# Optimization experiments

Hardware: AMD Instinct MI355X
Metric: run time of the kernel (lower is better)

Reference implementation:

```python
import jax, jax.numpy as jnp
from jax import lax
import numpy as np

B, S, E, HID = 16, 7, 64, 64
RES = (64, 64); D = RES[0] * RES[1]
XLOW, XHIGH = -0.5, 0.5
RLOW, RHIGH = float(np.sqrt(0.01)), float(np.sqrt(0.05))
PIXEL_MULT = 1.0; N_ITER = 3; TSOFT = 1.0 / float(np.sqrt(E))

def _build_grid():
    ranges = [np.linspace(XLOW, XHIGH, r) for r in RES]
    g = np.stack(np.meshgrid(*ranges, indexing='xy'), axis=-1)
    g = g.reshape(RES[0], RES[1], -1).reshape(1, -1, 2)
    return jnp.asarray(g, dtype=jnp.float32)

ABS_GRID = _build_grid()  # [1, D, 2]

def _ln(x, g, b):
    m = jnp.mean(x, -1, keepdims=True)
    v = jnp.mean(jnp.square(x - m), -1, keepdims=True)
    return (x - m) * lax.rsqrt(v + 1e-5) * g + b

def _forward(data, slot_noise, pos_rand, conv0_w, conv0_b, conv1_w, conv1_b, conv2_w, conv2_b,
             dataN_g, dataN_b, queryN_g, queryN_b, toK_w, toK_b, toV_w, toV_b, dense_w, dense_b,
             mlp1_w, mlp1_b, mlp2_w, mlp2_b, gru_wih, gru_whh, gru_bih, gru_bhh,
             alpha1_w, alpha1_b, alpha2_w, alpha2_b, final1_w, final1_b, final2_w, final2_b,
             slots_mu, slots_logsigma):
    dn = ('NCHW', 'OIHW', 'NCHW')
    def conv(x, w, b):
        return lax.conv_general_dilated(x, w, (1, 1), 'SAME', dimension_numbers=dn) + b[None, :, None, None]
    # CNN encoder: Conv-ReLU x3, 'same' padding, k=5
    x = jax.nn.relu(conv(data, conv0_w, conv0_b))
    x = jax.nn.relu(conv(x, conv1_w, conv1_b))
    x = jax.nn.relu(conv(x, conv2_w, conv2_b))
    enc = x.transpose(0, 2, 3, 1).reshape(B, D, HID)
    enc = _ln(enc, dataN_g, dataN_b)

    queries = slots_mu + jnp.exp(slots_logsigma) * slot_noise  # [B,S,E]
    # init_slots: faithful replication (source indexes the SLOT dim, and swaps rlow/rhigh)
    pos_scale = pos_rand.at[:, :2, :].add(-0.5)
    pos_scale = pos_scale.at[:, -1, :].set((RLOW - RHIGH) * pos_rand[:, -1, :] + RHIGH)

    encK = enc @ toK_w + toK_b  # [B,D,E]
    encV = enc @ toV_w + toV_b

    def init_mlp(y):
        y = _ln(y, queryN_g, queryN_b)
        return jax.nn.relu(y @ mlp1_w + mlp1_b) @ mlp2_w + mlp2_b

    def get_kv(ps):
        # per-slot relative grid: [B,S,D,2]
        rel = (ABS_GRID[:, None] - ps[:, :, None, :2]) / ps[:, :, -1][:, :, None, None]
        eg = PIXEL_MULT * (rel @ dense_w + dense_b)  # [B,S,D,E]
        return init_mlp(encK[:, None] + eg), init_mlp(encV[:, None] + eg)

    def att_wts(q, k):
        logits = jnp.einsum('bse,bsde->bsd', q, k) * TSOFT
        att = jax.nn.softmax(logits, axis=1)  # softmax over slots
        wts = att / jnp.sum(att, -1, keepdims=True) + 1e-8
        return att, wts

    def update_frames(wts):
        new_pos = jnp.einsum('bsd,de->bse', wts, ABS_GRID[0])  # [B,S,2]
        d2 = jnp.sum(jnp.square(ABS_GRID[:, None] - new_pos[:, :, None]), -1)  # [B,S,D]
        new_scale = jnp.sqrt(jnp.einsum('bsd,bsd->bs', wts, d2))
        return jnp.concatenate([new_pos, new_scale[..., None]], -1)

    def gru(xg, h):
        gi = xg @ gru_wih.T + gru_bih
        gh = h @ gru_whh.T + gru_bhh
        ir, iz, inn = jnp.split(gi, 3, -1)
        hr, hz, hn = jnp.split(gh, 3, -1)
        r = jax.nn.sigmoid(ir + hr)
        z = jax.nn.sigmoid(iz + hz)
        n = jnp.tanh(inn + r * hn)
        return (1.0 - z) * n + z * h

    for _ in range(N_ITER):
        keys, vals = get_kv(pos_scale)
        att, wts = att_wts(_ln(queries, queryN_g, queryN_b), keys)
        pos_scale = update_frames(wts)
        upd = jnp.einsum('bsd,bsde->bse', wts, vals)
        queries = gru(upd.reshape(-1, E), queries.reshape(-1, E)).reshape(B, S, E)

    keys, _ = get_kv(pos_scale)
    att, wts = att_wts(_ln(queries, queryN_g, queryN_b), keys)
    nps = update_frames(wts)
    alpha = jax.nn.sigmoid(jax.nn.relu(queries @ alpha1_w + alpha1_b) @ alpha2_w + alpha2_b)
    slot_feat = jax.nn.relu(queries @ final1_w + final1_b) @ final2_w + final2_b + nps
    return queries, att, slot_feat, alpha

def setup_inputs() -> dict:
    ks = jax.random.split(jax.random.key(0), 20)
    f32 = jnp.float32
    def rn(i, shape, s):
        return jax.random.normal(ks[i], shape, f32) * s
    inp = dict(
        data=jax.random.normal(ks[0], (B, 1, RES[0], RES[1]), f32),
        slot_noise=jax.random.normal(ks[1], (B, S, E), f32),
        pos_rand=jax.random.uniform(ks[2], (B, S, 3), dtype=f32),
        conv0_w=rn(3, (HID, 1, 5, 5), 0.2), conv0_b=jnp.zeros(HID, f32),
        conv1_w=rn(4, (HID, HID, 5, 5), 0.025), conv1_b=jnp.zeros(HID, f32),
        conv2_w=rn(5, (HID, HID, 5, 5), 0.025), conv2_b=jnp.zeros(HID, f32),
        dataN_g=jnp.ones(HID, f32), dataN_b=jnp.zeros(HID, f32),
        queryN_g=jnp.ones(E, f32), queryN_b=jnp.zeros(E, f32),
        toK_w=rn(6, (HID, E), 0.125), toK_b=jnp.zeros(E, f32),
        toV_w=rn(7, (HID, E), 0.125), toV_b=jnp.zeros(E, f32),
        dense_w=rn(8, (2, E), 0.7), dense_b=jnp.zeros(E, f32),
        mlp1_w=rn(9, (E, E), 0.125), mlp1_b=jnp.zeros(E, f32),
        mlp2_w=rn(10, (E, E), 0.125), mlp2_b=jnp.zeros(E, f32),
        gru_wih=rn(11, (3 * E, E), 0.125), gru_whh=rn(12, (3 * E, E), 0.125),
        gru_bih=jnp.zeros(3 * E, f32), gru_bhh=jnp.zeros(3 * E, f32),
        alpha1_w=rn(13, (E, 32), 0.125), alpha1_b=jnp.zeros(32, f32),
        alpha2_w=rn(14, (32, 1), 0.18), alpha2_b=jnp.zeros(1, f32),
        final1_w=rn(15, (E, HID), 0.125), final1_b=jnp.zeros(HID, f32),
        final2_w=rn(16, (HID, 3), 0.125), final2_b=jnp.zeros(3, f32),
        slots_mu=rn(17, (1, 1, E), 1.0),
        slots_logsigma=rn(18, (1, 1, E), 0.01),
    )
    return inp

def reference(data, slot_noise, pos_rand, conv0_w, conv0_b, conv1_w, conv1_b, conv2_w, conv2_b,
              dataN_g, dataN_b, queryN_g, queryN_b, toK_w, toK_b, toV_w, toV_b, dense_w, dense_b,
              mlp1_w, mlp1_b, mlp2_w, mlp2_b, gru_wih, gru_whh, gru_bih, gru_bhh,
              alpha1_w, alpha1_b, alpha2_w, alpha2_b, final1_w, final1_b, final2_w, final2_b,
              slots_mu, slots_logsigma):
    return _forward(data, slot_noise, pos_rand, conv0_w, conv0_b, conv1_w, conv1_b, conv2_w, conv2_b,
                    dataN_g, dataN_b, queryN_g, queryN_b, toK_w, toK_b, toV_w, toV_b, dense_w, dense_b,
                    mlp1_w, mlp1_b, mlp2_w, mlp2_b, gru_wih, gru_whh, gru_bih, gru_bhh,
                    alpha1_w, alpha1_b, alpha2_w, alpha2_b, final1_w, final1_b, final2_w, final2_b,
                    slots_mu, slots_logsigma)
```

## Files before the change

### kernel.cpp

```cpp
#include <hip/hip_runtime.h>
#include <cmath>


#define RLOW_F 0.1f
#define RHIGH_F 0.22360679774997896f

typedef __attribute__((ext_vector_type(8))) __bf16 bf16x8;
typedef __attribute__((ext_vector_type(4))) float f32x4;

__device__ __forceinline__ float wsum64(float v){
  #pragma unroll
  for (int off = 32; off > 0; off >>= 1) v += __shfl_xor(v, off, 64);
  return v;
}
__device__ __forceinline__ float rdlane(float v, int l){
  return __int_as_float(__builtin_amdgcn_readlane(__float_as_int(v), l));
}
__device__ __forceinline__ unsigned short bf16bits(float v){
  __bf16 h = (__bf16)v;
  return *reinterpret_cast<unsigned short*>(&h);
}

__device__ __forceinline__ void pp_core(int row, int e, float qv,
    float px, float py, float sc,
    const float* __restrict__ qg_, const float* __restrict__ qb_,
    const float* __restrict__ dw, const float* __restrict__ db,
    const float* __restrict__ mlp2w, const float* __restrict__ mlp2b,
    float* __restrict__ absc, float* __restrict__ w2qc,
    float* __restrict__ sum_att){
  float m = wsum64(qv) * (1.f/64.f);
  float d = qv - m;
  float var = wsum64(d*d) * (1.f/64.f);
  float qlnv = d * (1.0f/sqrtf(var + 1e-5f)) * qg_[e] + qb_[e];
  float A  = dw[e]      / sc;
  float Bv = dw[64 + e] / sc;
  absc[row*192 + e]       = A;
  absc[row*192 + 64 + e]  = Bv;
  absc[row*192 + 128 + e] = db[e] - px*A - py*Bv;
  float acc = 0.f;
  const float* wrow = mlp2w + e*64;
  for (int j = 0; j < 64; j++) acc = fmaf(wrow[j], rdlane(qlnv, j), acc);
  w2qc[row*68 + e] = acc;
  float c2 = wsum64(mlp2b[e] * qlnv);
  if (e == 0){ w2qc[row*68 + 64] = c2; sum_att[row] = 0.f; }
}

__global__ void k_prep(const float* __restrict__ noise, const float* __restrict__ prand,
                       const float* __restrict__ mu, const float* __restrict__ logsig,
                       const float* __restrict__ qg_, const float* __restrict__ qb_,
                       const float* __restrict__ dw, const float* __restrict__ db,
                       const float* __restrict__ mlp2w, const float* __restrict__ mlp2b,
                       float* __restrict__ queries, float* __restrict__ ps,
                       float* __restrict__ absc, float* __restrict__ w2qc,
                       float* __restrict__ sum_att, float* __restrict__ upd){
  int row = blockIdx.x;
  int e = threadIdx.x;
  int s = row % 7;
  float qv = mu[e] + expf(logsig[e]) * noise[row*64 + e];
  queries[row*64 + e] = qv;
  upd[row*64 + e] = 0.f;
  float pv = 0.f;
  if (e < 3){
    float pr = prand[row*3 + e];
    if (s < 2)       pv = pr - 0.5f;
    else if (s == 6) pv = (RLOW_F - RHIGH_F)*pr + RHIGH_F;
    else             pv = pr;
    ps[row*3 + e] = pv;
  }
  float px = rdlane(pv, 0), py = rdlane(pv, 1), sc = rdlane(pv, 2);
  pp_core(row, e, qv, px, py, sc, qg_, qb_, dw, db, mlp2w, mlp2b,
          absc, w2qc, sum_att);
}

__global__ __launch_bounds__(256) void k_conv0(const float* __restrict__ in,
                        const float* __restrict__ w, const float* __restrict__ bias,
                        unsigned short* __restrict__ out){
  int bi = blockIdx.x; int b = bi >> 6; int y = bi & 63;
  int t = threadIdx.x; int lane = t & 63; int xg = t >> 6;
  __shared__ float s_in[5*68];
  __shared__ float s_w[64*25];
  __shared__ float s_out[64*65];
  for (int i = t; i < 1600; i += 256) s_w[i] = w[i];
  for (int i = t; i < 340; i += 256){
    int r = i / 68, cx = i % 68;
    int yy = y + r - 2, gx = cx - 2;
    float v = 0.f;
    if (yy >= 0 && yy < 64 && gx >= 0 && gx < 64) v = in[(b*64 + yy)*64 + gx];
    s_in[r*68 + cx] = v;
  }
  __syncthreads();
  int o = lane;
  float bv = bias[o];
  float acc[16];
  #pragma unroll
  for (int k = 0; k < 16; k++) acc[k] = bv;
  #pragma unroll
  for (int ky = 0; ky < 5; ky++){
    float rv[20];
    const float4* p = reinterpret_cast<const float4*>(&s_in[ky*68 + xg*16]);
    #pragma unroll
    for (int q = 0; q < 5; q++){ float4 f = p[q]; rv[q*4]=f.x; rv[q*4+1]=f.y; rv[q*4+2]=f.z; rv[q*4+3]=f.w; }
    #pragma unroll
    for (int kx = 0; kx < 5; kx++){
      float wv = s_w[o*25 + ky*5 + kx];
      #pragma unroll
      for (int k = 0; k < 16; k++) acc[k] = fmaf(rv[k+kx], wv, acc[k]);
    }
  }
  #pragma unroll
  for (int k = 0; k < 16; k++) s_out[o*65 + xg*16 + k] = fmaxf(acc[k], 0.f);
  __syncthreads();
  for (int i = t; i < 4096; i += 256){
    int px = i >> 6, ch = i & 63;
    out[((size_t)(b*64 + y)*64 + px)*64 + ch] = bf16bits(s_out[ch*65 + px]);
  }
}

__global__ void k_packconv(const float* __restrict__ w, unsigned short* __restrict__ out){
  int idx = blockIdx.x*256 + threadIdx.x;
  if (idx >= 102400) return;
  int j = idx & 7;
  int l = (idx >> 3) & 63;
  int frag = idx >> 9;
  int nt = frag & 3;
  int ks = (frag >> 2) % 10;
  int dy = frag / 40;
  int q = l >> 4, cr = l & 15;
  int k = ks*32 + q*8 + j;
  int kx = k >> 6, ch = k & 63;
  int n = nt*16 + cr;
  out[idx] = bf16bits(w[((n*64 + ch)*5 + dy)*5 + kx]);
}

__global__ __launch_bounds__(256) void k_convm(const unsigned short* __restrict__ in_bf,
                        const unsigned short* __restrict__ wpack,
                        const float* __restrict__ bias,
                        const float* __restrict__ lng, const float* __restrict__ lnb,
                        unsigned short* __restrict__ out_bf, float* __restrict__ out_f,
                        int mode){
  int bi = blockIdx.x;
  int b = bi >> 4; int yg = bi & 15;
  int t = threadIdx.x; int wv = t >> 6; int l = t & 63;
  int q = l >> 4, cr = l & 15;
  int p0 = wv*16;

  __shared__ char lds[8*68*144];

  for (int ri = 0; ri < 8; ri++){
    int yy = yg*4 + ri - 2;
    bool rok = (yy >= 0 && yy < 64);
    const uint4* src = reinterpret_cast<const uint4*>(in_bf + (size_t)(b*64 + yy)*64*64);
    for (int i = t; i < 544; i += 256){
      int px = i >> 3, c8 = i & 7;
      uint4 v = {0u,0u,0u,0u};
      int gx = px - 2;
      if (rok && gx >= 0 && gx < 64) v = src[gx*8 + c8];
      *reinterpret_cast<uint4*>(&lds[ri*9792 + px*144 + c8*16]) = v;
    }
  }
  __syncthreads();

  f32x4 acc[4][4];
  #pragma unroll
  for (int r = 0; r < 4; r++)
    #pragma unroll
    for (int nt = 0; nt < 4; nt++) acc[r][nt] = (f32x4){0.f,0.f,0.f,0.f};

  const bf16x8* wp = reinterpret_cast<const bf16x8*>(wpack);
  for (int dy = 0; dy < 5; dy++){
    for (int ks = 0; ks < 10; ks++){
      bf16x8 Bf[4];
      int fbase = (dy*10 + ks)*4;
      #pragma unroll
      for (int nt = 0; nt < 4; nt++) Bf[nt] = wp[(fbase + nt)*64 + l];
      int aoff = (p0 + cr + (ks >> 1))*144 + (ks & 1)*64 + q*16;
      #pragma unroll
      for (int r = 0; r < 4; r++){
        bf16x8 a = *reinterpret_cast<const bf16x8*>(&lds[(r + dy)*9792 + aoff]);
        #pragma unroll
        for (int nt = 0; nt < 4; nt++)
          acc[r][nt] = __builtin_amdgcn_mfma_f32_16x16x32_bf16(a, Bf[nt], acc[r][nt], 0, 0, 0);
      }
    }
  }

  float bv[4];
  #pragma unroll
  for (int nt = 0; nt < 4; nt++) bv[nt] = bias[nt*16 + cr];

  if (mode == 0){
    #pragma unroll
    for (int r = 0; r < 4; r++){
      int y = yg*4 + r;
      #pragma unroll
      for (int reg = 0; reg < 4; reg++){
        int p = p0 + q*4 + reg;
        size_t base = ((size_t)(b*64 + y)*64 + p)*64;
        #pragma unroll
        for (int nt = 0; nt < 4; nt++)
          out_bf[base + nt*16 + cr] = bf16bits(fmaxf(acc[r][nt][reg] + bv[nt], 0.f));
      }
    }
  } else {
    float gv[4], bb[4];
    #pragma unroll
    for (int nt = 0; nt < 4; nt++){ gv[nt] = lng[nt*16 + cr]; bb[nt] = lnb[nt*16 + cr]; }
    #pragma unroll
    for (int r = 0; r < 4; r++){
      int y = yg*4 + r;
      #pragma unroll
      for (int reg = 0; reg < 4; reg++){
        int p = p0 + q*4 + reg;
        float v[4]; float s1 = 0.f, s2 = 0.f;
        #pragma unroll
        for (int nt = 0; nt < 4; nt++){
          v[nt] = fmaxf(acc[r][nt][reg] + bv[nt], 0.f);
          s1 += v[nt]; s2 += v[nt]*v[nt];
        }
        #pragma unroll
        for (int m = 1; m < 16; m <<= 1){ s1 += __shfl_xor(s1, m, 64); s2 += __shfl_xor(s2, m, 64); }
        float mean = s1 * (1.f/64.f);
        float var  = s2 * (1.f/64.f) - mean*mean;
        float rstd = 1.0f/sqrtf(var + 1e-5f);
        size_t base = ((size_t)b*4096 + y*64 + p)*64;
        #pragma unroll
        for (int nt = 0; nt < 4; nt++)
          out_f[base + nt*16 + cr] = (v[nt] - mean)*rstd*gv[nt] + bb[nt];
      }
    }
  }
}

__global__ void k_packw1(const float* __restrict__ w1, unsigned short* __restrict__ out){
  int idx = blockIdx.x*256 + threadIdx.x;
  int jj = idx & 7;
  int lane = (idx >> 3) & 63;
  int frag = idx >> 9;
  int ks = frag >> 2, nt = frag & 3;
  int q = lane >> 4, cr = lane & 15;
  int k = ks*32 + q*8 + jj;
  int n = nt*16 + cr;
  out[idx] = bf16bits(w1[k*64 + n]);
}

__global__ __launch_bounds__(256) void k_projm(const float* __restrict__ enc,
                       const unsigned short* __restrict__ kpack, const float* __restrict__ bk,
                       const unsigned short* __restrict__ vpack, const float* __restrict__ bvp,
                       float* __restrict__ K, float* __restrict__ V){
  int bi = blockIdx.x; int b = bi >> 6; int tile = bi & 63;
  int t = threadIdx.x; int wv = t >> 6; int l = t & 63;
  int q = l >> 4, cr = l & 15;
  int d0 = tile*64 + wv*16;

  const bf16x8* kp = reinterpret_cast<const bf16x8*>(kpack);
  const bf16x8* vp = reinterpret_cast<const bf16x8*>(vpack);
  bf16x8 KB[8], VB[8];
  #pragma unroll
  for (int f = 0; f < 8; f++){ KB[f] = kp[f*64 + l]; VB[f] = vp[f*64 + l]; }

  const float* er = enc + (size_t)(b*4096 + d0 + cr)*64;
  bf16x8 a0, a1;
  #pragma unroll
  for (int h = 0; h < 2; h++){
    const float4* e4 = reinterpret_cast<const float4*>(er + (h ? (32 + q*8) : (q*8)));
    #pragma unroll
    for (int p = 0; p < 2; p++){
      float4 e = e4[p];
      if (h == 0){ a0[p*4+0]=(__bf16)e.x; a0[p*4+1]=(__bf16)e.y; a0[p*4+2]=(__bf16)e.z; a0[p*4+3]=(__bf16)e.w; }
      else       { a1[p*4+0]=(__bf16)e.x; a1[p*4+1]=(__bf16)e.y; a1[p*4+2]=(__bf16)e.z; a1[p*4+3]=(__bf16)e.w; }
    }
  }

  f32x4 zero = {0.f,0.f,0.f,0.f};
  f32x4 aK[4], aV[4];
  #pragma unroll
  for (int nt = 0; nt < 4; nt++){
    aK[nt] = __builtin_amdgcn_mfma_f32_16x16x32_bf16(a0, KB[nt],     zero,   0, 0, 0);
    aK[nt] = __builtin_amdgcn_mfma_f32_16x16x32_bf16(a1, KB[4 + nt], aK[nt], 0, 0, 0);
    aV[nt] = __builtin_amdgcn_mfma_f32_16x16x32_bf16(a0, VB[nt],     zero,   0, 0, 0);
    aV[nt] = __builtin_amdgcn_mfma_f32_16x16x32_bf16(a1, VB[4 + nt], aV[nt], 0, 0, 0);
  }
  #pragma unroll
  for (int nt = 0; nt < 4; nt++){
    float bkv = bk[nt*16 + cr], bvv = bvp[nt*16 + cr];
    #pragma unroll
    for (int reg = 0; reg < 4; reg++){
      size_t base = ((size_t)b*4096 + d0 + q*4 + reg)*64 + nt*16 + cr;
      K[base] = aK[nt][reg] + bkv;
      V[base] = aV[nt][reg] + bvv;
    }
  }
}

__global__ __launch_bounds__(256) void k_attnK(const float* __restrict__ encX,
     const unsigned short* __restrict__ w1pack, const float* __restrict__ mlp1b,
     const float* __restrict__ absc, const float* __restrict__ qg_,
     const float* __restrict__ qb_, const float* __restrict__ w2qc,
     float* __restrict__ att, float* __restrict__ sum_att){
  int bi = blockIdx.x;
  int b = bi >> 6, tile = bi & 63;
  int t = threadIdx.x; int wv = t >> 6; int l = t & 63;
  int q = l >> 4, cr = l & 15;
  int m0 = tile*64 + wv*16;
  int drow = m0 + cr;

  __shared__ float s_log[7*64];
  __shared__ float s_absc[7*192];
  __shared__ float s_wq[7*68];
  for (int i = t; i < 1344; i += 256) s_absc[i] = absc[b*7*192 + i];
  for (int i = t; i < 476;  i += 256) s_wq[i]   = w2qc[b*7*68 + i];

  const bf16x8* wp = reinterpret_cast<const bf16x8*>(w1pack);
  bf16x8 Bf[8];
  #pragma unroll
  for (int f = 0; f < 8; f++) Bf[f] = wp[f*64 + l];

  const float* er = encX + (size_t)(b*4096 + drow)*64;
  float gx = -0.5f + (float)(drow & 63) * (1.f/63.f);
  float gy = -0.5f + (float)((drow >> 6) & 63) * (1.f/63.f);
  float xb[16], gq[16], bq[16];
  #pragma unroll
  for (int h = 0; h < 2; h++){
    int fb = h ? (32 + q*8) : (q*8);
    const float4* e4 = reinterpret_cast<const float4*>(er + fb);
    const float4* g4 = reinterpret_cast<const float4*>(qg_ + fb);
    const float4* b4 = reinterpret_cast<const float4*>(qb_ + fb);
    #pragma unroll
    for (int p = 0; p < 2; p++){
      float4 e = e4[p], gg = g4[p], bb = b4[p];
      int o = h*8 + p*4;
      xb[o+0]=e.x; xb[o+1]=e.y; xb[o+2]=e.z; xb[o+3]=e.w;
      gq[o+0]=gg.x; gq[o+1]=gg.y; gq[o+2]=gg.z; gq[o+3]=gg.w;
      bq[o+0]=bb.x; bq[o+1]=bb.y; bq[o+2]=bb.z; bq[o+3]=bb.w;
    }
  }
  float b1v[4];
  #pragma unroll
  for (int nt = 0; nt < 4; nt++) b1v[nt] = mlp1b[nt*16 + cr];
  __syncthreads();

  for (int s = 0; s < 7; s++){
    const float* Ac = s_absc + s*192;
    float x[16];
    #pragma unroll
    for (int h = 0; h < 2; h++){
      int fb = h ? (32 + q*8) : (q*8);
      const float4* A4 = reinterpret_cast<const float4*>(Ac + fb);
      const float4* B4 = reinterpret_cast<const float4*>(Ac + 64 + fb);
      const float4* C4 = reinterpret_cast<const float4*>(Ac + 128 + fb);
      #pragma unroll
      for (int p = 0; p < 2; p++){
        float4 Av = A4[p], Bv = B4[p], Cv = C4[p];
        int o = h*8 + p*4;
        x[o+0] = xb[o+0] + gx*Av.x + gy*Bv.x + Cv.x;
        x[o+1] = xb[o+1] + gx*Av.y + gy*Bv.y + Cv.y;
        x[o+2] = xb[o+2] + gx*Av.z + gy*Bv.z + Cv.z;
        x[o+3] = xb[o+3] + gx*Av.w + gy*Bv.w + Cv.w;
      }
    }
    float sum = 0.f;
    #pragma unroll
    for (int k = 0; k < 16; k++) sum += x[k];
    sum += __shfl_xor(sum, 16, 64); sum += __shfl_xor(sum, 32, 64);
    float m = sum * (1.f/64.f);
    float v = 0.f;
    #pragma unroll
    for (int k = 0; k < 16; k++){ float dd = x[k] - m; v += dd*dd; }
    v += __shfl_xor(v, 16, 64); v += __shfl_xor(v, 32, 64);
    float rstd = 1.0f/sqrtf(v * (1.f/64.f) + 1e-5f);

    bf16x8 a0, a1;
    #pragma unroll
    for (int k = 0; k < 8; k++)  a0[k] = (__bf16)((x[k]   - m)*rstd*gq[k]   + bq[k]);
    #pragma unroll
    for (int k = 0; k < 8; k++)  a1[k] = (__bf16)((x[8+k] - m)*rstd*gq[8+k] + bq[8+k]);

    f32x4 zero = {0.f, 0.f, 0.f, 0.f};
    f32x4 acc[4];
    #pragma unroll
    for (int nt = 0; nt < 4; nt++){
      acc[nt] = __builtin_amdgcn_mfma_f32_16x16x32_bf16(a0, Bf[nt],     zero,    0, 0, 0);
      acc[nt] = __builtin_amdgcn_mfma_f32_16x16x32_bf16(a1, Bf[4 + nt], acc[nt], 0, 0, 0);
    }

    float c2 = s_wq[s*68 + 64];
    float p[4] = {0.f, 0.f, 0.f, 0.f};
    #pragma unroll
    for (int nt = 0; nt < 4; nt++){
      float wqv = s_wq[s*68 + nt*16 + cr];
      #pragma unroll
      for (int reg = 0; reg < 4; reg++){
        float y = fmaxf(acc[nt][reg] + b1v[nt], 0.f);
        p[reg] = fmaf(y, wqv, p[reg]);
      }
    }
    #pragma unroll
    for (int reg = 0; reg < 4; reg++){
      #pragma unroll
      for (int off = 1; off < 16; off <<= 1) p[reg] += __shfl_xor(p[reg], off, 64);
    }
    if (cr == 0){
      #pragma unroll
      for (int reg = 0; reg < 4; reg++)
        s_log[s*64 + wv*16 + q*4 + reg] = (p[reg] + c2) * 0.125f;
    }
  }
  __syncthreads();

  if (t < 64){
    float lv[7];
    #pragma unroll
    for (int s = 0; s < 7; s++) lv[s] = s_log[s*64 + t];
    float mx = lv[0];
    #pragma unroll
    for (int s = 1; s < 7; s++) mx = fmaxf(mx, lv[s]);
    float sm = 0.f;
    #pragma unroll
    for (int s = 0; s < 7; s++){ lv[s] = expf(lv[s] - mx); sm += lv[s]; }
    float inv = 1.0f / sm;
    for (int s = 0; s < 7; s++){
      float a = lv[s] * inv;
      att[(size_t)(b*7+s)*4096 + tile*64 + t] = a;
      float ws = wsum64(a);
      if (t == 0) atomicAdd(&sum_att[b*7+s], ws);
    }
  }
}

__global__ __launch_bounds__(256) void k_attnV(const float* __restrict__ encX,
     const unsigned short* __restrict__ w1pack, const float* __restrict__ mlp1b,
     const float* __restrict__ absc, const float* __restrict__ qg_,
     const float* __restrict__ qb_, const float* __restrict__ att,
     const float* __restrict__ sum_att, float* __restrict__ upd){
  int bi = blockIdx.x;
  int b = bi >> 6, tile = bi & 63;
  int t = threadIdx.x; int wv = t >> 6; int l = t & 63;
  int q = l >> 4, cr = l & 15;
  int m0 = tile*64 + wv*16;
  int drow = m0 + cr;

  __shared__ float s_absc[7*192];
  __shared__ float s_att[7*64];
  __shared__ float s_upd[7*64];
  __shared__ float s_inv[7];
  for (int i = t; i < 1344; i += 256) s_absc[i] = absc[b*7*192 + i];
  for (int i = t; i < 448;  i += 256){
    s_att[i] = att[(size_t)(b*7 + (i >> 6))*4096 + tile*64 + (i & 63)];
    s_upd[i] = 0.f;
  }
  if (t < 7) s_inv[t] = 1.0f / sum_att[b*7 + t];

  const bf16x8* wp = reinterpret_cast<const bf16x8*>(w1pack);
  bf16x8 Bf[8];
  #pragma unroll
  for (int f = 0; f < 8; f++) Bf[f] = wp[f*64 + l];

  const float* er = encX + (size_t)(b*4096 + drow)*64;
  float gx = -0.5f + (float)(drow & 63) * (1.f/63.f);
  float gy = -0.5f + (float)((drow >> 6) & 63) * (1.f/63.f);
  float xb[16], gq[16], bq[16];
  #pragma unroll
  for (int h = 0; h < 2; h++){
    int fb = h ? (32 + q*8) : (q*8);
    const float4* e4 = reinterpret_cast<const float4*>(er + fb);
    const float4* g4 = reinterpret_cast<const float4*>(qg_ + fb);
    const float4* b4 = reinterpret_cast<const float4*>(qb_ + fb);
    #pragma unroll
    for (int p = 0; p < 2; p++){
      float4 e = e4[p], gg = g4[p], bb = b4[p];
      int o = h*8 + p*4;
      xb[o+0]=e.x; xb[o+1]=e.y; xb[o+2]=e.z; xb[o+3]=e.w;
      gq[o+0]=gg.x; gq[o+1]=gg.y; gq[o+2]=gg.z; gq[o+3]=gg.w;
      bq[o+0]=bb.x; bq[o+1]=bb.y; bq[o+2]=bb.z; bq[o+3]=bb.w;
    }
  }
  float b1v[4];
  #pragma unroll
  for (int nt = 0; nt < 4; nt++) b1v[nt] = mlp1b[nt*16 + cr];
  __syncthreads();

  for (int s = 0; s < 7; s++){
    const float* Ac = s_absc + s*192;
    float x[16];
    #pragma unroll
    for (int h = 0; h < 2; h++){
      int fb = h ? (32 + q*8) : (q*8);
      const float4* A4 = reinterpret_cast<const float4*>(Ac + fb);
      const float4* B4 = reinterpret_cast<const float4*>(Ac + 64 + fb);
      const float4* C4 = reinterpret_cast<const float4*>(Ac + 128 + fb);
      #pragma unroll
      for (int p = 0; p < 2; p++){
        float4 Av = A4[p], Bv = B4[p], Cv = C4[p];
        int o = h*8 + p*4;
        x[o+0] = xb[o+0] + gx*Av.x + gy*Bv.x + Cv.x;
        x[o+1] = xb[o+1] + gx*Av.y + gy*Bv.y + Cv.y;
        x[o+2] = xb[o+2] + gx*Av.z + gy*Bv.z + Cv.z;
        x[o+3] = xb[o+3] + gx*Av.w + gy*Bv.w + Cv.w;
      }
    }
    float sum = 0.f;
    #pragma unroll
    for (int k = 0; k < 16; k++) sum += x[k];
    sum += __shfl_xor(sum, 16, 64); sum += __shfl_xor(sum, 32, 64);
    float m = sum * (1.f/64.f);
    float v = 0.f;
    #pragma unroll
    for (int k = 0; k < 16; k++){ float dd = x[k] - m; v += dd*dd; }
    v += __shfl_xor(v, 16, 64); v += __shfl_xor(v, 32, 64);
    float rstd = 1.0f/sqrtf(v * (1.f/64.f) + 1e-5f);

    bf16x8 a0, a1;
    #pragma unroll
    for (int k = 0; k < 8; k++)  a0[k] = (__bf16)((x[k]   - m)*rstd*gq[k]   + bq[k]);
    #pragma unroll
    for (int k = 0; k < 8; k++)  a1[k] = (__bf16)((x[8+k] - m)*rstd*gq[8+k] + bq[8+k]);

    f32x4 zero = {0.f, 0.f, 0.f, 0.f};
    f32x4 acc[4];
    #pragma unroll
    for (int nt = 0; nt < 4; nt++){
      acc[nt] = __builtin_amdgcn_mfma_f32_16x16x32_bf16(a0, Bf[nt],     zero,    0, 0, 0);
      acc[nt] = __builtin_amdgcn_mfma_f32_16x16x32_bf16(a1, Bf[4 + nt], acc[nt], 0, 0, 0);
    }

    float rsa = s_inv[s];
    float wr[4];
    #pragma unroll
    for (int reg = 0; reg < 4; reg++)
      wr[reg] = fmaf(s_att[s*64 + wv*16 + q*4 + reg], rsa, 1e-8f);
    float pc[4];
    #pragma unroll
    for (int nt = 0; nt < 4; nt++){
      pc[nt] = 0.f;
      #pragma unroll
      for (int reg = 0; reg < 4; reg++)
        pc[nt] = fmaf(wr[reg], fmaxf(acc[nt][reg] + b1v[nt], 0.f), pc[nt]);
    }
    #pragma unroll
    for (int nt = 0; nt < 4; nt++){
      pc[nt] += __shfl_xor(pc[nt], 16, 64);
      pc[nt] += __shfl_xor(pc[nt], 32, 64);
    }
    if (q == 0){
      #pragma unroll
      for (int nt = 0; nt < 4; nt++)
        atomicAdd(&s_upd[s*64 + nt*16 + cr], pc[nt]);
    }
  }
  __syncthreads();
  for (int i = t; i < 448; i += 256)
    atomicAdd(&upd[b*448 + i], s_upd[i]);
}

__global__ void k_frames(const float* __restrict__ att, const float* __restrict__ sum_att,
                         float* __restrict__ psout, float* __restrict__ sumw){
  int bs = blockIdx.x; int t = threadIdx.x;
  float sa = sum_att[bs];
  float a0 = 0.f, ax = 0.f, ay = 0.f, a2 = 0.f;
  for (int d = t; d < 4096; d += 256){
    float wv = att[bs*4096 + d] / sa + 1e-8f;
    float gx = -0.5f + (float)(d & 63) * (1.f/63.f);
    float gy = -0.5f + (float)(d >> 6) * (1.f/63.f);
    a0 += wv; ax += wv*gx; ay += wv*gy; a2 += wv*(gx*gx + gy*gy);
  }
  __shared__ float red[4][4];
  int lane = t & 63, w = t >> 6;
  a0 = wsum64(a0); ax = wsum64(ax); ay = wsum64(ay); a2 = wsum64(a2);
  if (lane == 0){ red[w][0]=a0; red[w][1]=ax; red[w][2]=ay; red[w][3]=a2; }
  __syncthreads();
  if (t == 0){
    float W0=0,Wx=0,Wy=0,Wg=0;
    for (int k = 0; k < 4; k++){ W0+=red[k][0]; Wx+=red[k][1]; Wy+=red[k][2]; Wg+=red[k][3]; }
    float s2 = Wg - (Wx*Wx + Wy*Wy)*(2.f - W0);
    psout[bs*3+0] = Wx; psout[bs*3+1] = Wy; psout[bs*3+2] = sqrtf(fmaxf(s2, 0.f));
    sumw[bs] = W0;
  }
}

__global__ void k_gru(float* __restrict__ upd, float* __restrict__ queries,
                      const float* __restrict__ wih, const float* __restrict__ whh,
                      const float* __restrict__ bih, const float* __restrict__ bhh,
                      const float* __restrict__ mlp2w, const float* __restrict__ mlp2b,
                      const float* __restrict__ sumw, const float* __restrict__ ps,
                      const float* __restrict__ qg_, const float* __restrict__ qb_,
                      const float* __restrict__ dw, const float* __restrict__ db,
                      float* __restrict__ absc, float* __restrict__ w2qc,
                      float* __restrict__ sum_att){
  int row = blockIdx.x; int t = threadIdx.x;
  __shared__ float us[64], hs[64], xs[64], gis[192], ghs[192];
  if (t < 64){ us[t] = upd[row*64 + t]; hs[t] = queries[row*64 + t]; }
  __syncthreads();
  if (t < 64){
    float a = sumw[row] * mlp2b[t];
    for (int i = 0; i < 64; i++) a = fmaf(us[i], mlp2w[i*64 + t], a);
    xs[t] = a;
  }
  __syncthreads();
  float gi = bih[t], gh = bhh[t];
  for (int e = 0; e < 64; e++){
    gi = fmaf(wih[t*64 + e], xs[e], gi);
    gh = fmaf(whh[t*64 + e], hs[e], gh);
  }
  gis[t] = gi; ghs[t] = gh;
  __syncthreads();
  if (t < 64){
    float r = 1.0f/(1.0f + expf(-(gis[t]      + ghs[t])));
    float z = 1.0f/(1.0f + expf(-(gis[64+t]   + ghs[64+t])));
    float n = tanhf(gis[128+t] + r*ghs[128+t]);
    float newq = (1.0f - z)*n + z*hs[t];
    queries[row*64 + t] = newq;
    upd[row*64 + t] = 0.f;
    float px = ps[row*3], py = ps[row*3+1], sc = ps[row*3+2];
    pp_core(row, t, newq, px, py, sc, qg_, qb_, dw, db, mlp2w, mlp2b,
            absc, w2qc, sum_att);
  }
}

__global__ void k_final(const float* __restrict__ queries, const float* __restrict__ nps,
                        const float* __restrict__ a1w, const float* __restrict__ a1b,
                        const float* __restrict__ a2w, const float* __restrict__ a2b,
                        const float* __restrict__ f1w, const float* __restrict__ f1b,
                        const float* __restrict__ f2w, const float* __restrict__ f2b,
                        float* __restrict__ out){
  int bs = blockIdx.x; int e = threadIdx.x;
  __shared__ float qs[64], hf[64], ha[32];
  float q = queries[bs*64 + e];
  qs[e] = q;
  out[bs*64 + e] = q;
  __syncthreads();
  float accf = f1b[e];
  for (int i = 0; i < 64; i++) accf = fmaf(qs[i], f1w[i*64 + e], accf);
  hf[e] = fmaxf(accf, 0.f);
  if (e < 32){
    float acca = a1b[e];
    for (int i = 0; i < 64; i++) acca = fmaf(qs[i], a1w[i*32 + e], acca);
    ha[e] = fmaxf(acca, 0.f);
  }
  __syncthreads();
  if (e < 3){
    float sf = f2b[e];
    for (int o = 0; o < 64; o++) sf = fmaf(hf[o], f2w[o*3 + e], sf);
    out[465920 + bs*3 + e] = sf + nps[bs*3 + e];
  }
  if (e == 32){
    float al = a2b[0];
    for (int o = 0; o < 32; o++) al = fmaf(ha[o], a2w[o], al);
    out[466256 + bs] = 1.0f/(1.0f + expf(-al));
  }
}

extern "C" void kernel_launch(void* const* d_in, const int* in_sizes, int n_in,
                              void* d_out, int out_size, void* d_ws, size_t ws_size,
                              hipStream_t stream){
  const float* data        = (const float*)d_in[0];
  const float* slot_noise  = (const float*)d_in[1];
  const float* pos_rand    = (const float*)d_in[2];
  const float* conv0_w     = (const float*)d_in[3];
  const float* conv0_b     = (const float*)d_in[4];
  const float* conv1_w     = (const float*)d_in[5];
  const float* conv1_b     = (const float*)d_in[6];
  const float* conv2_w     = (const float*)d_in[7];
  const float* conv2_b     = (const float*)d_in[8];
  const float* dataN_g     = (const float*)d_in[9];
  const float* dataN_b     = (const float*)d_in[10];
  const float* queryN_g    = (const float*)d_in[11];
  const float* queryN_b    = (const float*)d_in[12];
  const float* toK_w       = (const float*)d_in[13];
  const float* toK_b       = (const float*)d_in[14];
  const float* toV_w       = (const float*)d_in[15];
  const float* toV_b       = (const float*)d_in[16];
  const float* dense_w     = (const float*)d_in[17];
  const float* dense_b     = (const float*)d_in[18];
  const float* mlp1_w      = (const float*)d_in[19];
  const float* mlp1_b      = (const float*)d_in[20];
  const float* mlp2_w      = (const float*)d_in[21];
  const float* mlp2_b      = (const float*)d_in[22];
  const float* gru_wih     = (const float*)d_in[23];
  const float* gru_whh     = (const float*)d_in[24];
  const float* gru_bih     = (const float*)d_in[25];
  const float* gru_bhh     = (const float*)d_in[26];
  const float* alpha1_w    = (const float*)d_in[27];
  const float* alpha1_b    = (const float*)d_in[28];
  const float* alpha2_w    = (const float*)d_in[29];
  const float* alpha2_b    = (const float*)d_in[30];
  const float* final1_w    = (const float*)d_in[31];
  const float* final1_b    = (const float*)d_in[32];
  const float* final2_w    = (const float*)d_in[33];
  const float* final2_b    = (const float*)d_in[34];
  const float* slots_mu    = (const float*)d_in[35];
  const float* slots_lsig  = (const float*)d_in[36];

  float* ws   = (float*)d_ws;
  float* bufA = ws;
  float* bufB = bufA + 4194304;
  float* bufC = bufB + 4194304;
  float* attw = bufC + 4194304;
  float* queries = attw + 458752;
  float* ps   = queries + 7168;
  float* absc = ps + 512;
  float* sum_att = absc + 21504;
  float* upd  = sum_att + 128;
  float* nps  = upd + 7168;
  float* w2qc = nps + 512;
  float* sumw = w2qc + 7616;
  unsigned short* w1pack = (unsigned short*)(sumw + 128);
  unsigned short* kpack  = w1pack + 4096;
  unsigned short* vpack  = kpack + 4096;
  unsigned short* wp1    = vpack + 4096;
  unsigned short* wp2    = wp1 + 102400;

  unsigned short* c0_bf = (unsigned short*)bufA;
  unsigned short* c1_bf = (unsigned short*)bufC;
  float* enc  = bufB;
  float* encK = bufA;
  float* encV = bufC;

  float* outq   = (float*)d_out;
  float* outatt = outq + 7168;

  k_prep<<<112, 64, 0, stream>>>(slot_noise, pos_rand, slots_mu, slots_lsig,
                                 queryN_g, queryN_b, dense_w, dense_b, mlp2_w, mlp2_b,
                                 queries, ps, absc, w2qc, sum_att, upd);
  k_packw1<<<16, 256, 0, stream>>>(mlp1_w, w1pack);
  k_packw1<<<16, 256, 0, stream>>>(toK_w, kpack);
  k_packw1<<<16, 256, 0, stream>>>(toV_w, vpack);
  k_packconv<<<400, 256, 0, stream>>>(conv1_w, wp1);
  k_packconv<<<400, 256, 0, stream>>>(conv2_w, wp2);
  k_conv0<<<1024, 256, 0, stream>>>(data, conv0_w, conv0_b, c0_bf);
  k_convm<<<256, 256, 0, stream>>>(c0_bf, wp1, conv1_b, nullptr, nullptr, c1_bf, nullptr, 0);
  k_convm<<<256, 256, 0, stream>>>(c1_bf, wp2, conv2_b, dataN_g, dataN_b, nullptr, enc, 1);
  k_projm<<<1024, 256, 0, stream>>>(enc, kpack, toK_b, vpack, toV_b, encK, encV);

  for (int p = 0; p < 4; p++){
    float* attp = (p == 3) ? outatt : attw;
    k_attnK<<<1024, 256, 0, stream>>>(encK, w1pack, mlp1_b, absc, queryN_g, queryN_b,
                                      w2qc, attp, sum_att);
    k_frames<<<112, 256, 0, stream>>>(attp, sum_att, (p == 3) ? nps : ps, sumw);
    if (p < 3){
      k_attnV<<<1024, 256, 0, stream>>>(encV, w1pack, mlp1_b, absc, queryN_g, queryN_b,
                                        attp, sum_att, upd);
      k_gru<<<112, 192, 0, stream>>>(upd, queries, gru_wih, gru_whh, gru_bih, gru_bhh,
                                     mlp2_w, mlp2_b, sumw, ps, queryN_g, queryN_b,
                                     dense_w, dense_b, absc, w2qc, sum_att);
    }
  }
  k_final<<<112, 64, 0, stream>>>(queries, nps, alpha1_w, alpha1_b, alpha2_w, alpha2_b,
                                  final1_w, final1_b, final2_w, final2_b, outq);
}
```

Before: 565.7 us.

## Fuse frame-moment reduction into attention kernel and store K/V in bf16

Removes the separate k_frames kernel. k_attnK now reduces the per-slot weighted moments (sum, x, y, r^2) within each block and accumulates them with atomics. The new slot position and scale are computed analytically in k_gru and k_final, and W0 and the 1e-8 term become closed-form constants. Encoded K and V are also stored as bf16, which halves the bytes the attention kernels read on every iteration. The cost is bf16 rounding of K/V, a reformulated reduction with a different summation order, and hardcoded constants that depend on the grid resolution.

```diff
diff --git a/kernel.cpp b/kernel.cpp
--- a/kernel.cpp
+++ b/kernel.cpp
@@ -4,6 +4,8 @@
 
 #define RLOW_F 0.1f
 #define RHIGH_F 0.22360679774997896f
+#define W0CONST 1.00004096f
+#define SR2 704.3386243f
 
 typedef __attribute__((ext_vector_type(8))) __bf16 bf16x8;
 typedef __attribute__((ext_vector_type(4))) float f32x4;
@@ -26,8 +28,7 @@
     const float* __restrict__ qg_, const float* __restrict__ qb_,
     const float* __restrict__ dw, const float* __restrict__ db,
     const float* __restrict__ mlp2w, const float* __restrict__ mlp2b,
-    float* __restrict__ absc, float* __restrict__ w2qc,
-    float* __restrict__ sum_att){
+    float* __restrict__ absc, float* __restrict__ w2qc){
   float m = wsum64(qv) * (1.f/64.f);
   float d = qv - m;
   float var = wsum64(d*d) * (1.f/64.f);
@@ -42,7 +43,7 @@
   for (int j = 0; j < 64; j++) acc = fmaf(wrow[j], rdlane(qlnv, j), acc);
   w2qc[row*68 + e] = acc;
   float c2 = wsum64(mlp2b[e] * qlnv);
-  if (e == 0){ w2qc[row*68 + 64] = c2; sum_att[row] = 0.f; }
+  if (e == 0) w2qc[row*68 + 64] = c2;
 }
 
 __global__ void k_prep(const float* __restrict__ noise, const float* __restrict__ prand,
@@ -52,13 +53,14 @@
                        const float* __restrict__ mlp2w, const float* __restrict__ mlp2b,
                        float* __restrict__ queries, float* __restrict__ ps,
                        float* __restrict__ absc, float* __restrict__ w2qc,
-                       float* __restrict__ sum_att, float* __restrict__ upd){
+                       float* __restrict__ accF, float* __restrict__ upd){
   int row = blockIdx.x;
   int e = threadIdx.x;
   int s = row % 7;
   float qv = mu[e] + expf(logsig[e]) * noise[row*64 + e];
   queries[row*64 + e] = qv;
   upd[row*64 + e] = 0.f;
+  if (e < 4) accF[row*4 + e] = 0.f;
   float pv = 0.f;
   if (e < 3){
     float pr = prand[row*3 + e];
@@ -68,8 +70,7 @@
     ps[row*3 + e] = pv;
   }
   float px = rdlane(pv, 0), py = rdlane(pv, 1), sc = rdlane(pv, 2);
-  pp_core(row, e, qv, px, py, sc, qg_, qb_, dw, db, mlp2w, mlp2b,
-          absc, w2qc, sum_att);
+  pp_core(row, e, qv, px, py, sc, qg_, qb_, dw, db, mlp2w, mlp2b, absc, w2qc);
 }
 
 __global__ __launch_bounds__(256) void k_conv0(const float* __restrict__ in,
@@ -90,10 +91,10 @@
   }
   __syncthreads();
   int o = lane;
-  float bv = bias[o];
+  float bvv = bias[o];
   float acc[16];
   #pragma unroll
-  for (int k = 0; k < 16; k++) acc[k] = bv;
+  for (int k = 0; k < 16; k++) acc[k] = bvv;
   #pragma unroll
   for (int ky = 0; ky < 5; ky++){
     float rv[20];
@@ -184,9 +185,9 @@
     }
   }
 
-  float bv[4];
-  #pragma unroll
-  for (int nt = 0; nt < 4; nt++) bv[nt] = bias[nt*16 + cr];
+  float bvv[4];
+  #pragma unroll
+  for (int nt = 0; nt < 4; nt++) bvv[nt] = bias[nt*16 + cr];
 
   if (mode == 0){
     #pragma unroll
@@ -198,7 +199,7 @@
         size_t base = ((size_t)(b*64 + y)*64 + p)*64;
         #pragma unroll
         for (int nt = 0; nt < 4; nt++)
-          out_bf[base + nt*16 + cr] = bf16bits(fmaxf(acc[r][nt][reg] + bv[nt], 0.f));
+          out_bf[base + nt*16 + cr] = bf16bits(fmaxf(acc[r][nt][reg] + bvv[nt], 0.f));
       }
     }
   } else {
@@ -214,7 +215,7 @@
         float v[4]; float s1 = 0.f, s2 = 0.f;
         #pragma unroll
         for (int nt = 0; nt < 4; nt++){
-          v[nt] = fmaxf(acc[r][nt][reg] + bv[nt], 0.f);
+          v[nt] = fmaxf(acc[r][nt][reg] + bvv[nt], 0.f);
           s1 += v[nt]; s2 += v[nt]*v[nt];
         }
         #pragma unroll
@@ -246,7 +247,7 @@
 __global__ __launch_bounds__(256) void k_projm(const float* __restrict__ enc,
                        const unsigned short* __restrict__ kpack, const float* __restrict__ bk,
                        const unsigned short* __restrict__ vpack, const float* __restrict__ bvp,
-                       float* __restrict__ K, float* __restrict__ V){
+                       unsigned short* __restrict__ K, unsigned short* __restrict__ V){
   int bi = blockIdx.x; int b = bi >> 6; int tile = bi & 63;
   int t = threadIdx.x; int wv = t >> 6; int l = t & 63;
   int q = l >> 4, cr = l & 15;
@@ -286,17 +287,17 @@
     #pragma unroll
     for (int reg = 0; reg < 4; reg++){
       size_t base = ((size_t)b*4096 + d0 + q*4 + reg)*64 + nt*16 + cr;
-      K[base] = aK[nt][reg] + bkv;
-      V[base] = aV[nt][reg] + bvv;
-    }
-  }
-}
-
-__global__ __launch_bounds__(256) void k_attnK(const float* __restrict__ encX,
+      K[base] = bf16bits(aK[nt][reg] + bkv);
+      V[base] = bf16bits(aV[nt][reg] + bvv);
+    }
+  }
+}
+
+__global__ __launch_bounds__(256) void k_attnK(const unsigned short* __restrict__ encX,
      const unsigned short* __restrict__ w1pack, const float* __restrict__ mlp1b,
      const float* __restrict__ absc, const float* __restrict__ qg_,
      const float* __restrict__ qb_, const float* __restrict__ w2qc,
-     float* __restrict__ att, float* __restrict__ sum_att){
+     float* __restrict__ att, float* __restrict__ accF){
   int bi = blockIdx.x;
   int b = bi >> 6, tile = bi & 63;
   int t = threadIdx.x; int wv = t >> 6; int l = t & 63;
@@ -315,21 +316,25 @@
   #pragma unroll
   for (int f = 0; f < 8; f++) Bf[f] = wp[f*64 + l];
 
-  const float* er = encX + (size_t)(b*4096 + drow)*64;
+  const unsigned short* er = encX + (size_t)(b*4096 + drow)*64;
   float gx = -0.5f + (float)(drow & 63) * (1.f/63.f);
   float gy = -0.5f + (float)((drow >> 6) & 63) * (1.f/63.f);
   float xb[16], gq[16], bq[16];
+  {
+    bf16x8 ea = *reinterpret_cast<const bf16x8*>(er + q*8);
+    bf16x8 eb = *reinterpret_cast<const bf16x8*>(er + 32 + q*8);
+    #pragma unroll
+    for (int i = 0; i < 8; i++){ xb[i] = (float)ea[i]; xb[8+i] = (float)eb[i]; }
+  }
   #pragma unroll
   for (int h = 0; h < 2; h++){
     int fb = h ? (32 + q*8) : (q*8);
-    const float4* e4 = reinterpret_cast<const float4*>(er + fb);
     const float4* g4 = reinterpret_cast<const float4*>(qg_ + fb);
     const float4* b4 = reinterpret_cast<const float4*>(qb_ + fb);
     #pragma unroll
     for (int p = 0; p < 2; p++){
-      float4 e = e4[p], gg = g4[p], bb = b4[p];
+      float4 gg = g4[p], bb = b4[p];
       int o = h*8 + p*4;
-      xb[o+0]=e.x; xb[o+1]=e.y; xb[o+2]=e.z; xb[o+3]=e.w;
       gq[o+0]=gg.x; gq[o+1]=gg.y; gq[o+2]=gg.z; gq[o+3]=gg.w;
       bq[o+0]=bb.x; bq[o+1]=bb.y; bq[o+2]=bb.z; bq[o+3]=bb.w;
     }
@@ -418,20 +423,48 @@
     #pragma unroll
     for (int s = 0; s < 7; s++){ lv[s] = expf(lv[s] - mx); sm += lv[s]; }
     float inv = 1.0f / sm;
+    #pragma unroll
     for (int s = 0; s < 7; s++){
       float a = lv[s] * inv;
+      s_log[s*64 + t] = a;
       att[(size_t)(b*7+s)*4096 + tile*64 + t] = a;
-      float ws = wsum64(a);
-      if (t == 0) atomicAdd(&sum_att[b*7+s], ws);
-    }
-  }
-}
-
-__global__ __launch_bounds__(256) void k_attnV(const float* __restrict__ encX,
+    }
+  }
+  __syncthreads();
+
+  if (t < 224){
+    int s = t >> 5, r = t & 31;
+    float a1 = s_log[s*64 + r];
+    float a2 = s_log[s*64 + r + 32];
+    float gx1 = -0.5f + (float)r * (1.f/63.f);
+    float gx2 = -0.5f + (float)(r + 32) * (1.f/63.f);
+    float gyc = -0.5f + (float)tile * (1.f/63.f);
+    float gy2c = gyc*gyc;
+    float w0 = a1 + a2;
+    float w1 = a1*gx1 + a2*gx2;
+    float w2 = w0*gyc;
+    float w3 = a1*(gx1*gx1 + gy2c) + a2*(gx2*gx2 + gy2c);
+    #pragma unroll
+    for (int m = 1; m < 32; m <<= 1){
+      w0 += __shfl_xor(w0, m, 64);
+      w1 += __shfl_xor(w1, m, 64);
+      w2 += __shfl_xor(w2, m, 64);
+      w3 += __shfl_xor(w3, m, 64);
+    }
+    if (r == 0){
+      atomicAdd(&accF[(b*7+s)*4 + 0], w0);
+      atomicAdd(&accF[(b*7+s)*4 + 1], w1);
+      atomicAdd(&accF[(b*7+s)*4 + 2], w2);
+      atomicAdd(&accF[(b*7+s)*4 + 3], w3);
+    }
+  }
+}
+
+__global__ __launch_bounds__(256) void k_attnV(const unsigned short* __restrict__ encX,
      const unsigned short* __restrict__ w1pack, const float* __restrict__ mlp1b,
      const float* __restrict__ absc, const float* __restrict__ qg_,
      const float* __restrict__ qb_, const float* __restrict__ att,
-     const float* __restrict__ sum_att, float* __restrict__ upd){
+     const float* __restrict__ accF, float* __restrict__ upd){
   int bi = blockIdx.x;
   int b = bi >> 6, tile = bi & 63;
   int t = threadIdx.x; int wv = t >> 6; int l = t & 63;
@@ -448,28 +481,32 @@
     s_att[i] = att[(size_t)(b*7 + (i >> 6))*4096 + tile*64 + (i & 63)];
     s_upd[i] = 0.f;
   }
-  if (t < 7) s_inv[t] = 1.0f / sum_att[b*7 + t];
+  if (t < 7) s_inv[t] = 1.0f / accF[(b*7 + t)*4];
 
   const bf16x8* wp = reinterpret_cast<const bf16x8*>(w1pack);
   bf16x8 Bf[8];
   #pragma unroll
   for (int f = 0; f < 8; f++) Bf[f] = wp[f*64 + l];
 
-  const float* er = encX + (size_t)(b*4096 + drow)*64;
+  const unsigned short* er = encX + (size_t)(b*4096 + drow)*64;
   float gx = -0.5f + (float)(drow & 63) * (1.f/63.f);
   float gy = -0.5f + (float)((drow >> 6) & 63) * (1.f/63.f);
   float xb[16], gq[16], bq[16];
+  {
+    bf16x8 ea = *reinterpret_cast<const bf16x8*>(er + q*8);
+    bf16x8 eb = *reinterpret_cast<const bf16x8*>(er + 32 + q*8);
+    #pragma unroll
+    for (int i = 0; i < 8; i++){ xb[i] = (float)ea[i]; xb[8+i] = (float)eb[i]; }
+  }
   #pragma unroll
   for (int h = 0; h < 2; h++){
     int fb = h ? (32 + q*8) : (q*8);
-    const float4* e4 = reinterpret_cast<const float4*>(er + fb);
     const float4* g4 = reinterpret_cast<const float4*>(qg_ + fb);
     const float4* b4 = reinterpret_cast<const float4*>(qb_ + fb);
     #pragma unroll
     for (int p = 0; p < 2; p++){
-      float4 e = e4[p], gg = g4[p], bb = b4[p];
+      float4 gg = g4[p], bb = b4[p];
       int o = h*8 + p*4;
-      xb[o+0]=e.x; xb[o+1]=e.y; xb[o+2]=e.z; xb[o+3]=e.w;
       gq[o+0]=gg.x; gq[o+1]=gg.y; gq[o+2]=gg.z; gq[o+3]=gg.w;
       bq[o+0]=bb.x; bq[o+1]=bb.y; bq[o+2]=bb.z; bq[o+3]=bb.w;
     }
@@ -552,46 +589,30 @@
     atomicAdd(&upd[b*448 + i], s_upd[i]);
 }
 
-__global__ void k_frames(const float* __restrict__ att, const float* __restrict__ sum_att,
-                         float* __restrict__ psout, float* __restrict__ sumw){
-  int bs = blockIdx.x; int t = threadIdx.x;
-  float sa = sum_att[bs];
-  float a0 = 0.f, ax = 0.f, ay = 0.f, a2 = 0.f;
-  for (int d = t; d < 4096; d += 256){
-    float wv = att[bs*4096 + d] / sa + 1e-8f;
-    float gx = -0.5f + (float)(d & 63) * (1.f/63.f);
-    float gy = -0.5f + (float)(d >> 6) * (1.f/63.f);
-    a0 += wv; ax += wv*gx; ay += wv*gy; a2 += wv*(gx*gx + gy*gy);
-  }
-  __shared__ float red[4][4];
-  int lane = t & 63, w = t >> 6;
-  a0 = wsum64(a0); ax = wsum64(ax); ay = wsum64(ay); a2 = wsum64(a2);
-  if (lane == 0){ red[w][0]=a0; red[w][1]=ax; red[w][2]=ay; red[w][3]=a2; }
-  __syncthreads();
-  if (t == 0){
-    float W0=0,Wx=0,Wy=0,Wg=0;
-    for (int k = 0; k < 4; k++){ W0+=red[k][0]; Wx+=red[k][1]; Wy+=red[k][2]; Wg+=red[k][3]; }
-    float s2 = Wg - (Wx*Wx + Wy*Wy)*(2.f - W0);
-    psout[bs*3+0] = Wx; psout[bs*3+1] = Wy; psout[bs*3+2] = sqrtf(fmaxf(s2, 0.f));
-    sumw[bs] = W0;
-  }
-}
-
 __global__ void k_gru(float* __restrict__ upd, float* __restrict__ queries,
                       const float* __restrict__ wih, const float* __restrict__ whh,
                       const float* __restrict__ bih, const float* __restrict__ bhh,
                       const float* __restrict__ mlp2w, const float* __restrict__ mlp2b,
-                      const float* __restrict__ sumw, const float* __restrict__ ps,
+                      float* __restrict__ accF, float* __restrict__ ps,
                       const float* __restrict__ qg_, const float* __restrict__ qb_,
                       const float* __restrict__ dw, const float* __restrict__ db,
-                      float* __restrict__ absc, float* __restrict__ w2qc,
-                      float* __restrict__ sum_att){
+                      float* __restrict__ absc, float* __restrict__ w2qc){
   int row = blockIdx.x; int t = threadIdx.x;
   __shared__ float us[64], hs[64], xs[64], gis[192], ghs[192];
+  __shared__ float s_ps3[3];
   if (t < 64){ us[t] = upd[row*64 + t]; hs[t] = queries[row*64 + t]; }
+  if (t == 64){
+    float sa = accF[row*4+0];
+    float ax = accF[row*4+1], ay = accF[row*4+2], ar2 = accF[row*4+3];
+    float isa = 1.0f/sa;
+    float Wx = ax*isa, Wy = ay*isa;
+    float Wg = ar2*isa + 1e-8f*SR2;
+    float s2 = Wg - (Wx*Wx + Wy*Wy)*(2.f - W0CONST);
+    s_ps3[0] = Wx; s_ps3[1] = Wy; s_ps3[2] = sqrtf(fmaxf(s2, 0.f));
+  }
   __syncthreads();
   if (t < 64){
-    float a = sumw[row] * mlp2b[t];
+    float a = W0CONST * mlp2b[t];
     for (int i = 0; i < 64; i++) a = fmaf(us[i], mlp2w[i*64 + t], a);
     xs[t] = a;
   }
@@ -610,13 +631,14 @@
     float newq = (1.0f - z)*n + z*hs[t];
     queries[row*64 + t] = newq;
     upd[row*64 + t] = 0.f;
-    float px = ps[row*3], py = ps[row*3+1], sc = ps[row*3+2];
-    pp_core(row, t, newq, px, py, sc, qg_, qb_, dw, db, mlp2w, mlp2b,
-            absc, w2qc, sum_att);
-  }
-}
-
-__global__ void k_final(const float* __restrict__ queries, const float* __restrict__ nps,
+    if (t < 4) accF[row*4 + t] = 0.f;
+    if (t < 3) ps[row*3 + t] = s_ps3[t];
+    pp_core(row, t, newq, s_ps3[0], s_ps3[1], s_ps3[2],
+            qg_, qb_, dw, db, mlp2w, mlp2b, absc, w2qc);
+  }
+}
+
+__global__ void k_final(const float* __restrict__ queries, const float* __restrict__ accF,
                         const float* __restrict__ a1w, const float* __restrict__ a1b,
                         const float* __restrict__ a2w, const float* __restrict__ a2b,
                         const float* __restrict__ f1w, const float* __restrict__ f1b,
@@ -640,7 +662,13 @@
   if (e < 3){
     float sf = f2b[e];
     for (int o = 0; o < 64; o++) sf = fmaf(hf[o], f2w[o*3 + e], sf);
-    out[465920 + bs*3 + e] = sf + nps[bs*3 + e];
+    float sa = accF[bs*4+0], ax = accF[bs*4+1], ay = accF[bs*4+2], ar2 = accF[bs*4+3];
+    float isa = 1.0f/sa;
+    float Wx = ax*isa, Wy = ay*isa;
+    float Wg = ar2*isa + 1e-8f*SR2;
+    float s2 = Wg - (Wx*Wx + Wy*Wy)*(2.f - W0CONST);
+    float nv = (e == 0) ? Wx : ((e == 1) ? Wy : sqrtf(fmaxf(s2, 0.f)));
+    out[465920 + bs*3 + e] = sf + nv;
   }
   if (e == 32){
     float al = a2b[0];
@@ -698,12 +726,10 @@
   float* queries = attw + 458752;
   float* ps   = queries + 7168;
   float* absc = ps + 512;
-  float* sum_att = absc + 21504;
-  float* upd  = sum_att + 128;
-  float* nps  = upd + 7168;
-  float* w2qc = nps + 512;
-  float* sumw = w2qc + 7616;
-  unsigned short* w1pack = (unsigned short*)(sumw + 128);
+  float* accF = absc + 21504;
+  float* upd  = accF + 512;
+  float* w2qc = upd + 7168;
+  unsigned short* w1pack = (unsigned short*)(w2qc + 7616);
   unsigned short* kpack  = w1pack + 4096;
   unsigned short* vpack  = kpack + 4096;
   unsigned short* wp1    = vpack + 4096;
@@ -711,16 +737,16 @@
 
   unsigned short* c0_bf = (unsigned short*)bufA;
   unsigned short* c1_bf = (unsigned short*)bufC;
-  float* enc  = bufB;
-  float* encK = bufA;
-  float* encV = bufC;
+  float* enc = bufB;
+  unsigned short* encK = (unsigned short*)bufA;
+  unsigned short* encV = (unsigned short*)bufC;
 
   float* outq   = (float*)d_out;
   float* outatt = outq + 7168;
 
   k_prep<<<112, 64, 0, stream>>>(slot_noise, pos_rand, slots_mu, slots_lsig,
                                  queryN_g, queryN_b, dense_w, dense_b, mlp2_w, mlp2_b,
-                                 queries, ps, absc, w2qc, sum_att, upd);
+                                 queries, ps, absc, w2qc, accF, upd);
   k_packw1<<<16, 256, 0, stream>>>(mlp1_w, w1pack);
   k_packw1<<<16, 256, 0, stream>>>(toK_w, kpack);
   k_packw1<<<16, 256, 0, stream>>>(toV_w, vpack);
@@ -734,16 +760,16 @@
   for (int p = 0; p < 4; p++){
     float* attp = (p == 3) ? outatt : attw;
     k_attnK<<<1024, 256, 0, stream>>>(encK, w1pack, mlp1_b, absc, queryN_g, queryN_b,
-                                      w2qc, attp, sum_att);
-    k_frames<<<112, 256, 0, stream>>>(attp, sum_att, (p == 3) ? nps : ps, sumw);
+                                      w2qc, attp, accF);
     if (p < 3){
       k_attnV<<<1024, 256, 0, stream>>>(encV, w1pack, mlp1_b, absc, queryN_g, queryN_b,
-                                        attp, sum_att, upd);
+                                        attp, accF, upd);
       k_gru<<<112, 192, 0, stream>>>(upd, queries, gru_wih, gru_whh, gru_bih, gru_bhh,
-                                     mlp2_w, mlp2_b, sumw, ps, queryN_g, queryN_b,
-                                     dense_w, dense_b, absc, w2qc, sum_att);
-    }
-  }
-  k_final<<<112, 64, 0, stream>>>(queries, nps, alpha1_w, alpha1_b, alpha2_w, alpha2_b,
+                                     mlp2_w, mlp2_b, accF, ps, queryN_g, queryN_b,
+                                     dense_w, dense_b, absc, w2qc);
+    }
+  }
+  k_final<<<112, 64, 0, stream>>>(queries, accF,
+                                  alpha1_w, alpha1_b, alpha2_w, alpha2_b,
                                   final1_w, final1_b, final2_w, final2_b, outq);
 }
```

Result: faster. 535.2 us (-5.4%).
